# Performance work log

Measured on AMD Instinct MI355X. Metric: run time of the kernel, lower is better.

Reference implementation:

```python
import jax, jax.numpy as jnp
import numpy as np

B, S, D, H = 2, 2048, 1024, 16
HD = D // H  # head_dim = 64


def setup_inputs() -> dict:
    key = jax.random.key(0)
    ks = jax.random.split(key, 9)
    xav = float(np.sqrt(6.0 / (D + D)))  # xavier_uniform bound for square matrices
    def lin_w(k):
        return jax.random.uniform(k, (D, D), jnp.float32, -xav, xav)
    return {
        "x": jax.random.normal(ks[0], (B, S, D), jnp.float32),
        "mask": jnp.ones((B, S), jnp.int32),
        "Wq": lin_w(ks[1]), "bq": jnp.zeros((D,), jnp.float32),
        "Wk": lin_w(ks[2]), "bk": jnp.zeros((D,), jnp.float32),
        "Wv": lin_w(ks[3]), "bv": jnp.zeros((D,), jnp.float32),
        "Wo": lin_w(ks[4]), "bo": jnp.zeros((D,), jnp.float32),
    }


def reference(x, mask, Wq, bq, Wk, bk, Wv, bv, Wo, bo):
    # Linear projections (torch Linear: y = x @ W.T + b)
    q = x @ Wq.T + bq
    k = x @ Wk.T + bk
    v = x @ Wv.T + bv
    # [B, S, D] -> [B, H, S, HD]
    q = q.reshape(B, S, H, HD).transpose(0, 2, 1, 3)
    k = k.reshape(B, S, H, HD).transpose(0, 2, 1, 3)
    v = v.reshape(B, S, H, HD).transpose(0, 2, 1, 3)
    scores = jnp.einsum("bhqd,bhkd->bhqk", q, k) / jnp.sqrt(jnp.float32(HD))
    # mask [B, S] -> [B, 1, 1, S]; masked_fill where mask == 0
    m = mask[:, None, None, :]
    scores = jnp.where(m == 0, jnp.float32(-1e9), scores)
    attn = jax.nn.softmax(scores, axis=-1)
    # dropout in eval mode = identity
    out = jnp.einsum("bhqk,bhkd->bhqd", attn, v)
    out = out.transpose(0, 2, 1, 3).reshape(B, S, D)
    return out @ Wo.T + bo
```

## Files before the change

kernel.cpp:

```cpp
#include <hip/hip_runtime.h>
#include <stdint.h>

#define B_   2
#define S_   2048
#define D_   1024
#define H_   16
#define HD_  64
#define NTOK (B_ * S_)

typedef unsigned short u16;
typedef __bf16 bf16x8 __attribute__((ext_vector_type(8)));
typedef float  f32x4  __attribute__((ext_vector_type(4)));
typedef u16    u16x4  __attribute__((ext_vector_type(4)));
typedef unsigned int u32x2 __attribute__((ext_vector_type(2)));

#define QSCALE 0.180336880f
#define MAXC 4.0f

#if __has_builtin(__builtin_amdgcn_exp2f)
#define EXP2(x) __builtin_amdgcn_exp2f(x)
#else
#define EXP2(x) exp2f(x)
#endif

#define OFF_FLAG ((size_t)0)
#define OFF_BIAS ((size_t)64)
#define OFF_MB   ((size_t)32768)
#define OFF_MF   ((size_t)49152)
#define OFF_X    ((size_t)65536)
#define SZ_X     ((size_t)NTOK * D_ * 2)
#define OFF_W    (OFF_X + SZ_X)
#define SZ_W     ((size_t)D_ * D_ * 2)
#define OFF_Q    (OFF_W + 4 * SZ_W)
#define SZ_T     SZ_X
#define OFF_K2   (OFF_Q + SZ_T)
#define OFF_VT   (OFF_K2 + SZ_T)
#define OFF_AO   (OFF_VT + SZ_T)

__device__ __forceinline__ float bf2f(u16 h) {
    union { uint32_t u; float f; } c; c.u = ((uint32_t)h) << 16; return c.f;
}
__device__ __forceinline__ u16 f2bf(float f) {
    union { float f; uint32_t u; } c; c.f = f;
    uint32_t r = c.u + 0x7fffu + ((c.u >> 16) & 1u);
    return (u16)(r >> 16);
}
__device__ __forceinline__ void glds16(const u16* g, u16* l) {
    __builtin_amdgcn_global_load_lds(
        (const __attribute__((address_space(1))) uint32_t*)g,
        (__attribute__((address_space(3))) uint32_t*)l,
        16, 0, 0);
}
__device__ __forceinline__ f32x4 mfma16(bf16x8 a, bf16x8 b, f32x4 c) {
    return __builtin_amdgcn_mfma_f32_16x16x32_bf16(a, b, c, 0, 0, 0);
}
__device__ __forceinline__ uint32_t pk_bf_trunc(float f0, float f1) {
    return __builtin_amdgcn_perm(__builtin_bit_cast(uint32_t, f1),
                                 __builtin_bit_cast(uint32_t, f0), 0x07060302u);
}
__device__ __forceinline__ void plswap32(uint32_t& a, uint32_t& b) {
#if __has_builtin(__builtin_amdgcn_permlane32_swap)
    u32x2 r = __builtin_amdgcn_permlane32_swap(a, b, false, false);
    a = r[0]; b = r[1];
#else
    asm volatile("s_nop 1\n\tv_permlane32_swap_b32 %0, %1\n\ts_nop 1"
                 : "+v"(a), "+v"(b));
#endif
}
__device__ __forceinline__ void plswap16(uint32_t& a, uint32_t& b) {
#if __has_builtin(__builtin_amdgcn_permlane16_swap)
    u32x2 r = __builtin_amdgcn_permlane16_swap(a, b, false, false);
    a = r[0]; b = r[1];
#else
    asm volatile("s_nop 1\n\tv_permlane16_swap_b32 %0, %1\n\ts_nop 1"
                 : "+v"(a), "+v"(b));
#endif
}

__global__ void convert_kernel(const void* x, const void* wq, const void* wk,
                               const void* wv, const void* wo,
                               const void* bq, const void* bk, const void* bv,
                               const void* bo, const int* mask, char* ws) {
    __shared__ int s_ok;
    const int tid = threadIdx.x;
    if (tid == 0) s_ok = 1;
    __syncthreads();
    {
        const u16* p = (const u16*)wq;
        bool bad = false;
        for (int j = 0; j < 8; ++j) {
            float v = bf2f(p[(tid * 8 + j) * 2]);
            if (!(v > -1.0f && v < 1.0f)) bad = true;
        }
        if (bad) s_ok = 0;
    }
    __syncthreads();
    const int is_bf16 = s_ok;
    if (blockIdx.x == 0 && tid == 0) *(int*)(ws + OFF_FLAG) = is_bf16;

    const uint32_t NX = (uint32_t)NTOK * D_;
    const uint32_t NW = (uint32_t)D_ * D_;
    if (!is_bf16) {
        u16* Xd = (u16*)(ws + OFF_X);
        u16* Wd = (u16*)(ws + OFF_W);
        for (uint32_t i = blockIdx.x * 256u + tid; i < NX + 4 * NW;
             i += gridDim.x * 256u) {
            const void* src; uint32_t si; u16* dst;
            if (i < NX) { src = x; si = i; dst = Xd + i; }
            else {
                uint32_t j = i - NX;
                uint32_t w = j >> 20; si = j & (NW - 1u);
                src = (w == 0) ? wq : (w == 1) ? wk : (w == 2) ? wv : wo;
                dst = Wd + j;
            }
            *dst = f2bf(((const float*)src)[si]);
        }
    }
    float* Bd = (float*)(ws + OFF_BIAS);
    float* Mbd = (float*)(ws + OFF_MB);
    int* MFd = (int*)(ws + OFF_MF);
    const uint32_t NB = 4u * D_;
    const uint32_t total2 = NB + (uint32_t)NTOK + B_ * 32;
    for (uint32_t i = blockIdx.x * 256u + tid; i < total2;
         i += gridDim.x * 256u) {
        if (i < NB) {
            uint32_t w = i >> 10; uint32_t si = i & (D_ - 1u);
            const void* src = (w == 0) ? bq : (w == 1) ? bk : (w == 2) ? bv : bo;
            Bd[i] = is_bf16 ? bf2f(((const u16*)src)[si]) : ((const float*)src)[si];
        } else if (i < NB + (uint32_t)NTOK) {
            uint32_t j = i - NB;
            Mbd[j] = (mask[j] == 0) ? -1.0e9f : 0.0f;
        } else {
            uint32_t f = i - NB - (uint32_t)NTOK;
            uint32_t bb = f >> 5, kt = f & 31;
            int any = 0;
            for (int e = 0; e < 64; ++e)
                any |= (mask[bb * S_ + kt * 64 + e] == 0);
            MFd[f] = any;
        }
    }
}

__global__ void qkv_gemm(char* ws, const void* x, const void* wq,
                         const void* wk, const void* wv) {
    __shared__ alignas(16) u16 As[128 * 32];
    __shared__ alignas(16) u16 Bs[128 * 32];
    const int z = blockIdx.z;
    const int is_bf16 = *(const int*)(ws + OFF_FLAG);
    const u16* X = is_bf16 ? (const u16*)x : (const u16*)(ws + OFF_X);
    const u16* W;
    if (is_bf16) W = (z == 0) ? (const u16*)wq : (z == 1) ? (const u16*)wk : (const u16*)wv;
    else         W = (const u16*)(ws + OFF_W + (size_t)z * SZ_W);
    const float* bias = (const float*)(ws + OFF_BIAS) + z * D_;
    u16* Qd  = (u16*)(ws + OFF_Q);
    u16* Kd  = (u16*)(ws + OFF_K2);
    u16* Vtd = (u16*)(ws + OFF_VT);

    const int tid = threadIdx.x, lane = tid & 63, wave = tid >> 6;
    const int wm = (wave & 1) * 64, wn = (wave >> 1) * 64;
    const int lr = lane & 15, quad = lane >> 4;
    const int srow = tid >> 2;
    const int scol = (((tid & 3) ^ ((tid >> 3) & 3)) * 8);
    const int rd_off = (quad ^ ((lr >> 1) & 3)) * 8;

    const u16* Araw; const u16* Braw; int m0, n0;
    if (z < 2) { Araw = W; Braw = X; m0 = blockIdx.x * 128; n0 = blockIdx.y * 128; }
    else       { Araw = X; Braw = W; m0 = blockIdx.y * 128; n0 = blockIdx.x * 128; }

    f32x4 acc[4][4];
#pragma unroll
    for (int i = 0; i < 4; i++)
#pragma unroll
        for (int j = 0; j < 4; j++) acc[i][j] = (f32x4){0.f, 0.f, 0.f, 0.f};

    const u16* Ag0 = Araw + (size_t)(m0 + srow)      * D_ + scol;
    const u16* Ag1 = Araw + (size_t)(m0 + srow + 64) * D_ + scol;
    const u16* Bg0 = Braw + (size_t)(n0 + srow)      * D_ + scol;
    const u16* Bg1 = Braw + (size_t)(n0 + srow + 64) * D_ + scol;

    for (int k0 = 0; k0 < D_; k0 += 32) {
        glds16(Ag0 + k0, &As[tid * 8]);
        glds16(Ag1 + k0, &As[2048 + tid * 8]);
        glds16(Bg0 + k0, &Bs[tid * 8]);
        glds16(Bg1 + k0, &Bs[2048 + tid * 8]);
        __syncthreads();
        bf16x8 a[4], b[4];
#pragma unroll
        for (int i = 0; i < 4; i++) a[i] = *(const bf16x8*)&As[(wm + i * 16 + lr) * 32 + rd_off];
#pragma unroll
        for (int j = 0; j < 4; j++) b[j] = *(const bf16x8*)&Bs[(wn + j * 16 + lr) * 32 + rd_off];
#pragma unroll
        for (int i = 0; i < 4; i++)
#pragma unroll
            for (int j = 0; j < 4; j++) acc[i][j] = mfma16(a[i], b[j], acc[i][j]);
        __syncthreads();
    }

    if (z < 2) {
        u16* dst0 = (z == 0) ? Qd : Kd;
        const float sc_ = (z == 0) ? QSCALE : 1.0f;
#pragma unroll
        for (int i = 0; i < 4; i++) {
            const int fb = m0 + wm + i * 16 + quad * 4;
            const f32x4 b4 = *(const f32x4*)&bias[fb];
            const int h = fb >> 6, hd0 = fb & 63;
#pragma unroll
            for (int j = 0; j < 4; j++) {
                const int tok = n0 + wn + j * 16 + lr;
                const int bb = tok >> 11, s = tok & 2047;
                u16x4 pk;
#pragma unroll
                for (int r = 0; r < 4; r++) pk[r] = f2bf((acc[i][j][r] + b4[r]) * sc_);
                *(u16x4*)&dst0[(((size_t)(bb * H_ + h)) * S_ + s) * HD_ + hd0] = pk;
            }
        }
    } else {
#pragma unroll
        for (int i = 0; i < 4; i++) {
            const int row_b = m0 + wm + i * 16 + quad * 4;
            const int bb = row_b >> 11, s0 = row_b & 2047;
#pragma unroll
            for (int j = 0; j < 4; j++) {
                const int col = n0 + wn + j * 16 + lr;
                const float bv_ = bias[col];
                const int h = col >> 6, hd = col & 63;
                u16x4 pk;
#pragma unroll
                for (int r = 0; r < 4; r++) pk[r] = f2bf(acc[i][j][r] + bv_);
                *(u16x4*)&Vtd[(((size_t)(bb * H_ + h)) * HD_ + hd) * S_ + s0] = pk;
            }
        }
    }
}

__global__ void __launch_bounds__(256, 2)
attn_kernel(char* ws) {
    __shared__ alignas(16) char smem[32768];

    const u16* Qb  = (const u16*)(ws + OFF_Q);
    const u16* Kb  = (const u16*)(ws + OFF_K2);
    const u16* Vtb = (const u16*)(ws + OFF_VT);
    const float* Mb = (const float*)(ws + OFF_MB);
    const int* MF = (const int*)(ws + OFF_MF);
    u16* AO = (u16*)(ws + OFF_AO);

    const int tid = threadIdx.x, lane = tid & 63, wave = tid >> 6;
    const int lin = blockIdx.x;
    const int work = (lin & 7) * 64 + (lin >> 3);
    const int bh = work >> 4, b = bh >> 4, h = bh & 15;
    const int qb = (work & 15) * 128 + wave * 32;
    const int lr = lane & 15, quad = lane >> 4;
    const int sx = lr & 7;

    const u16* Qbh = Qb  + (size_t)bh * S_ * HD_;
    const u16* Kbh = Kb  + (size_t)bh * S_ * HD_;
    const u16* Vbh = Vtb + (size_t)bh * HD_ * S_;
    const float* Mbb = Mb + b * S_;
    const int* MFb = MF + b * 32;

    u16* Ks0  = (u16*)(smem);
    u16* Vts0 = (u16*)(smem + 8192);
    u16* Ks1  = (u16*)(smem + 16384);
    u16* Vts1 = (u16*)(smem + 24576);

    const int st_r = tid >> 3;
    const int st_c = (tid & 7) ^ (st_r & 7);
    const u16* Kst = Kbh + (size_t)st_r * HD_ + st_c * 8;
    const u16* Vst = Vbh + (size_t)st_r * S_ + st_c * 8;

    bf16x8 qf[2][2];
#pragma unroll
    for (int s = 0; s < 2; ++s)
#pragma unroll
        for (int hf = 0; hf < 2; ++hf)
            qf[s][hf] = *(const bf16x8*)&Qbh[(size_t)(qb + s * 16 + lr) * HD_ + hf * 32 + quad * 8];

    bf16x8 ones8;
#pragma unroll
    for (int i = 0; i < 8; ++i) ones8[i] = (__bf16)1.0f;

    const f32x4 initm = (f32x4){-MAXC, -MAXC, -MAXC, -MAXC};

    f32x4 oacc[2][4], lacc[2];
#pragma unroll
    for (int s = 0; s < 2; ++s) {
        lacc[s] = (f32x4){0.f, 0.f, 0.f, 0.f};
#pragma unroll
        for (int j = 0; j < 4; ++j) oacc[s][j] = (f32x4){0.f, 0.f, 0.f, 0.f};
    }

    auto STAGE = [&](int it2, u16* Kd, u16* Vd) {
        const u16* kg = Kst + (size_t)it2 * 64 * HD_;
        const u16* vg = Vst + it2 * 64;
#pragma unroll
        for (int t = 0; t < 2; ++t) {
            glds16(kg + (size_t)t * 32 * HD_, &Kd[(t * 256 + tid) * 8]);
            glds16(vg + (size_t)t * 32 * S_,  &Vd[(t * 256 + tid) * 8]);
        }
    };

    auto COMPUTE = [&](int it, const u16* Ks, const u16* Vts) {
        const int k0 = it * 64;
        f32x4 sc[2][4];
        __builtin_amdgcn_s_setprio(1);
#pragma unroll
        for (int j = 0; j < 4; ++j) {
            const int krow = (j * 16 + lr) * 64;
            bf16x8 kfA = *(const bf16x8*)&Ks[krow + ((quad    ) ^ sx) * 8];
            bf16x8 kfB = *(const bf16x8*)&Ks[krow + ((quad + 4) ^ sx) * 8];
#pragma unroll
            for (int s = 0; s < 2; ++s) {
                f32x4 t0 = mfma16(kfA, qf[s][0], initm);
                sc[s][j] = mfma16(kfB, qf[s][1], t0);
            }
        }
        __builtin_amdgcn_s_setprio(0);
        if (MFb[it]) {
#pragma unroll
            for (int j = 0; j < 4; ++j) {
                const f32x4 mb = *(const f32x4*)&Mbb[k0 + j * 16 + quad * 4];
#pragma unroll
                for (int s = 0; s < 2; ++s) sc[s][j] += mb;
            }
        }
        bf16x8 vf[4][2];
#pragma unroll
        for (int j2 = 0; j2 < 4; ++j2) {
            const int vrow = (j2 * 16 + lr) * 64;
            vf[j2][0] = *(const bf16x8*)&Vts[vrow + ((quad    ) ^ sx) * 8];
            vf[j2][1] = *(const bf16x8*)&Vts[vrow + ((quad + 4) ^ sx) * 8];
        }

#pragma unroll
        for (int s = 0; s < 2; ++s) {
            uint32_t ulo[4], uhi[4];
#pragma unroll
            for (int j = 0; j < 4; ++j) {
                f32x4 p;
#pragma unroll
                for (int r = 0; r < 4; ++r) p[r] = EXP2(sc[s][j][r]);
                ulo[j] = pk_bf_trunc(p[0], p[1]);
                uhi[j] = pk_bf_trunc(p[2], p[3]);
            }
            bf16x8 pf[2];
#pragma unroll
            for (int half = 0; half < 2; ++half) {
                uint32_t x0 = ulo[2 * half], y0 = ulo[2 * half + 1];
                uint32_t x1 = uhi[2 * half], y1 = uhi[2 * half + 1];
                plswap32(x0, y0); plswap16(x0, y0);
                plswap32(x1, y1); plswap16(x1, y1);
                union { uint32_t u[4]; bf16x8 v; } cvt;
                cvt.u[0] = x0;
                cvt.u[1] = x1;
                cvt.u[2] = y0;
                cvt.u[3] = y1;
                pf[half] = cvt.v;
            }
            __builtin_amdgcn_s_setprio(1);
            lacc[s] = mfma16(ones8, pf[0], lacc[s]);
            lacc[s] = mfma16(ones8, pf[1], lacc[s]);
#pragma unroll
            for (int j2 = 0; j2 < 4; ++j2) {
                oacc[s][j2] = mfma16(vf[j2][0], pf[0], oacc[s][j2]);
                oacc[s][j2] = mfma16(vf[j2][1], pf[1], oacc[s][j2]);
            }
            __builtin_amdgcn_s_setprio(0);
        }
    };

    STAGE(0, Ks0, Vts0);
    for (int itp = 0; itp < 16; ++itp) {
        const int itA = 2 * itp, itB = 2 * itp + 1;
        __syncthreads();
        STAGE(itB, Ks1, Vts1);
        COMPUTE(itA, Ks0, Vts0);
        __syncthreads();
        if (itA + 2 < 32) STAGE(itA + 2, Ks0, Vts0);
        COMPUTE(itB, Ks1, Vts1);
    }

#pragma unroll
    for (int s = 0; s < 2; ++s) {
        const float linv = 1.0f / lacc[s][0];
        const int q = qb + s * 16 + lr;
        u16* dst = AO + (size_t)(b * S_ + q) * D_ + h * HD_ + quad * 4;
#pragma unroll
        for (int j2 = 0; j2 < 4; ++j2) {
            u16x4 pk;
#pragma unroll
            for (int r = 0; r < 4; ++r) pk[r] = f2bf(oacc[s][j2][r] * linv);
            *(u16x4*)&dst[j2 * 16] = pk;
        }
    }
}

__global__ void out_gemm(char* ws, const void* wo, void* dout) {
    __shared__ alignas(16) u16 As[128 * 32];
    __shared__ alignas(16) u16 Bs[64 * 32];
    const int is_bf16 = *(const int*)(ws + OFF_FLAG);
    const u16* A  = (const u16*)(ws + OFF_AO);
    const u16* Bt = is_bf16 ? (const u16*)wo : (const u16*)(ws + OFF_W + 3 * SZ_W);
    const float* bias = (const float*)(ws + OFF_BIAS) + 3 * D_;

    const int tid = threadIdx.x, lane = tid & 63, wave = tid >> 6;
    const int wm = (wave & 1) * 64, wn = (wave >> 1) * 32;
    const int m0 = blockIdx.y * 128, n0 = blockIdx.x * 64;
    const int lr = lane & 15, quad = lane >> 4;
    const int srow = tid >> 2;
    const int scol = (((tid & 3) ^ ((tid >> 3) & 3)) * 8);
    const int rd_off = (quad ^ ((lr >> 1) & 3)) * 8;

    f32x4 acc[4][2];
#pragma unroll
    for (int i = 0; i < 4; i++)
#pragma unroll
        for (int j = 0; j < 2; j++) acc[i][j] = (f32x4){0.f, 0.f, 0.f, 0.f};

    const u16* Ag0 = A  + (size_t)(m0 + srow)      * D_ + scol;
    const u16* Ag1 = A  + (size_t)(m0 + srow + 64) * D_ + scol;
    const u16* Bg0 = Bt + (size_t)(n0 + srow)      * D_ + scol;

    for (int k0 = 0; k0 < D_; k0 += 32) {
        glds16(Ag0 + k0, &As[tid * 8]);
        glds16(Ag1 + k0, &As[2048 + tid * 8]);
        glds16(Bg0 + k0, &Bs[tid * 8]);
        __syncthreads();
        bf16x8 a[4], b[2];
#pragma unroll
        for (int i = 0; i < 4; i++) a[i] = *(const bf16x8*)&As[(wm + i * 16 + lr) * 32 + rd_off];
#pragma unroll
        for (int j = 0; j < 2; j++) b[j] = *(const bf16x8*)&Bs[(wn + j * 16 + lr) * 32 + rd_off];
#pragma unroll
        for (int i = 0; i < 4; i++)
#pragma unroll
            for (int j = 0; j < 2; j++) acc[i][j] = mfma16(a[i], b[j], acc[i][j]);
        __syncthreads();
    }
#pragma unroll
    for (int i = 0; i < 4; i++) {
        const int row_b = m0 + wm + i * 16 + quad * 4;
#pragma unroll
        for (int j = 0; j < 2; j++) {
            const int col = n0 + wn + j * 16 + lr;
            const float bv_ = bias[col];
#pragma unroll
            for (int r = 0; r < 4; r++) {
                const int row = row_b + r;
                const float v = acc[i][j][r] + bv_;
                const size_t idx = (size_t)row * D_ + col;
                if (is_bf16) ((u16*)dout)[idx] = f2bf(v);
                else         ((float*)dout)[idx] = v;
            }
        }
    }
}

extern "C" void kernel_launch(void* const* d_in, const int* in_sizes, int n_in,
                              void* d_out, int out_size, void* d_ws, size_t ws_size,
                              hipStream_t stream) {
    (void)in_sizes; (void)n_in; (void)out_size; (void)ws_size;
    const void* x  = d_in[0];
    const int* mask = (const int*)d_in[1];
    const void* wq = d_in[2]; const void* bq = d_in[3];
    const void* wk = d_in[4]; const void* bk = d_in[5];
    const void* wv = d_in[6]; const void* bv = d_in[7];
    const void* wo = d_in[8]; const void* bo = d_in[9];
    char* ws = (char*)d_ws;

    convert_kernel<<<dim3(2048), dim3(256), 0, stream>>>(x, wq, wk, wv, wo,
                                                         bq, bk, bv, bo, mask, ws);
    qkv_gemm<<<dim3(8, 32, 3), dim3(256), 0, stream>>>(ws, x, wq, wk, wv);
    attn_kernel<<<dim3(512), dim3(256), 0, stream>>>(ws);
    out_gemm<<<dim3(16, 32), dim3(256), 0, stream>>>(ws, wo, d_out);
}
```

Before: 206.5 us.

## Double-buffer LDS in projection GEMMs, remap blocks per XCD, vectorize output stores

Both projection GEMMs now use two LDS buffers, so the global-to-LDS loads for the next K slice are issued while the current slice is computed. The loop is unrolled by two and drops one barrier per K step. Blocks are launched on a flat grid and remapped so consecutive blocks on the same XCD share token tiles, which is meant to improve L2 reuse. out_gemm swaps operand roles (Wo as A, activations as B) so the epilogue can write vectorized 4-wide rows with a vector bias load. Launch bounds are added, and the doubled LDS may limit occupancy.

```diff
diff --git a/kernel.cpp b/kernel.cpp
--- a/kernel.cpp
+++ b/kernel.cpp
@@ -141,11 +141,17 @@
     }
 }
 
-__global__ void qkv_gemm(char* ws, const void* x, const void* wq,
-                         const void* wk, const void* wv) {
-    __shared__ alignas(16) u16 As[128 * 32];
-    __shared__ alignas(16) u16 Bs[128 * 32];
-    const int z = blockIdx.z;
+__global__ void __launch_bounds__(256, 3)
+qkv_gemm(char* ws, const void* x, const void* wq,
+         const void* wk, const void* wv) {
+    __shared__ alignas(16) u16 As[2][128 * 32];
+    __shared__ alignas(16) u16 Bs[2][128 * 32];
+    const int lin = blockIdx.x;
+    const int xcd = lin & 7, slot = lin >> 3;
+    const int zx = slot >> 2, ly = slot & 3;
+    const int z = zx >> 3, xt = zx & 7;
+    const int yt = xcd * 4 + ly;
+
     const int is_bf16 = *(const int*)(ws + OFF_FLAG);
     const u16* X = is_bf16 ? (const u16*)x : (const u16*)(ws + OFF_X);
     const u16* W;
@@ -164,8 +170,8 @@
     const int rd_off = (quad ^ ((lr >> 1) & 3)) * 8;
 
     const u16* Araw; const u16* Braw; int m0, n0;
-    if (z < 2) { Araw = W; Braw = X; m0 = blockIdx.x * 128; n0 = blockIdx.y * 128; }
-    else       { Araw = X; Braw = W; m0 = blockIdx.y * 128; n0 = blockIdx.x * 128; }
+    if (z < 2) { Araw = W; Braw = X; m0 = xt * 128; n0 = yt * 128; }
+    else       { Araw = X; Braw = W; m0 = yt * 128; n0 = xt * 128; }
 
     f32x4 acc[4][4];
 #pragma unroll
@@ -178,22 +184,32 @@
     const u16* Bg0 = Braw + (size_t)(n0 + srow)      * D_ + scol;
     const u16* Bg1 = Braw + (size_t)(n0 + srow + 64) * D_ + scol;
 
-    for (int k0 = 0; k0 < D_; k0 += 32) {
-        glds16(Ag0 + k0, &As[tid * 8]);
-        glds16(Ag1 + k0, &As[2048 + tid * 8]);
-        glds16(Bg0 + k0, &Bs[tid * 8]);
-        glds16(Bg1 + k0, &Bs[2048 + tid * 8]);
+    auto STAGE = [&](int k0, u16* Ad, u16* Bd2) {
+        glds16(Ag0 + k0, &Ad[tid * 8]);
+        glds16(Ag1 + k0, &Ad[2048 + tid * 8]);
+        glds16(Bg0 + k0, &Bd2[tid * 8]);
+        glds16(Bg1 + k0, &Bd2[2048 + tid * 8]);
+    };
+    auto COMPUTE = [&](const u16* Ad, const u16* Bd2) {
+        bf16x8 a[4], b[4];
+#pragma unroll
+        for (int i = 0; i < 4; i++) a[i] = *(const bf16x8*)&Ad[(wm + i * 16 + lr) * 32 + rd_off];
+#pragma unroll
+        for (int j = 0; j < 4; j++) b[j] = *(const bf16x8*)&Bd2[(wn + j * 16 + lr) * 32 + rd_off];
+#pragma unroll
+        for (int i = 0; i < 4; i++)
+#pragma unroll
+            for (int j = 0; j < 4; j++) acc[i][j] = mfma16(a[i], b[j], acc[i][j]);
+    };
+
+    STAGE(0, As[0], Bs[0]);
+    for (int kp = 0; kp < 16; ++kp) {
         __syncthreads();
-        bf16x8 a[4], b[4];
-#pragma unroll
-        for (int i = 0; i < 4; i++) a[i] = *(const bf16x8*)&As[(wm + i * 16 + lr) * 32 + rd_off];
-#pragma unroll
-        for (int j = 0; j < 4; j++) b[j] = *(const bf16x8*)&Bs[(wn + j * 16 + lr) * 32 + rd_off];
-#pragma unroll
-        for (int i = 0; i < 4; i++)
-#pragma unroll
-            for (int j = 0; j < 4; j++) acc[i][j] = mfma16(a[i], b[j], acc[i][j]);
+        STAGE(kp * 64 + 32, As[1], Bs[1]);
+        COMPUTE(As[0], Bs[0]);
         __syncthreads();
+        if (kp < 15) STAGE(kp * 64 + 64, As[0], Bs[0]);
+        COMPUTE(As[1], Bs[1]);
     }
 
     if (z < 2) {
@@ -394,17 +410,23 @@
     }
 }
 
-__global__ void out_gemm(char* ws, const void* wo, void* dout) {
-    __shared__ alignas(16) u16 As[128 * 32];
-    __shared__ alignas(16) u16 Bs[64 * 32];
+__global__ void __launch_bounds__(256, 2)
+out_gemm(char* ws, const void* wo, void* dout) {
+    __shared__ alignas(16) u16 As[2][128 * 32];
+    __shared__ alignas(16) u16 Bs[2][64 * 32];
     const int is_bf16 = *(const int*)(ws + OFF_FLAG);
-    const u16* A  = (const u16*)(ws + OFF_AO);
-    const u16* Bt = is_bf16 ? (const u16*)wo : (const u16*)(ws + OFF_W + 3 * SZ_W);
+    const u16* A  = is_bf16 ? (const u16*)wo : (const u16*)(ws + OFF_W + 3 * SZ_W);
+    const u16* Bt = (const u16*)(ws + OFF_AO);
     const float* bias = (const float*)(ws + OFF_BIAS) + 3 * D_;
+
+    const int lin = blockIdx.x;
+    const int xcd = lin & 7, slot = lin >> 3;
+    const int ty = xcd * 8 + (slot >> 3);
+    const int fx = slot & 7;
+    const int m0 = fx * 128, n0 = ty * 64;
 
     const int tid = threadIdx.x, lane = tid & 63, wave = tid >> 6;
     const int wm = (wave & 1) * 64, wn = (wave >> 1) * 32;
-    const int m0 = blockIdx.y * 128, n0 = blockIdx.x * 64;
     const int lr = lane & 15, quad = lane >> 4;
     const int srow = tid >> 2;
     const int scol = (((tid & 3) ^ ((tid >> 3) & 3)) * 8);
@@ -420,36 +442,51 @@
     const u16* Ag1 = A  + (size_t)(m0 + srow + 64) * D_ + scol;
     const u16* Bg0 = Bt + (size_t)(n0 + srow)      * D_ + scol;
 
-    for (int k0 = 0; k0 < D_; k0 += 32) {
-        glds16(Ag0 + k0, &As[tid * 8]);
-        glds16(Ag1 + k0, &As[2048 + tid * 8]);
-        glds16(Bg0 + k0, &Bs[tid * 8]);
+    auto STAGE = [&](int k0, u16* Ad, u16* Bd2) {
+        glds16(Ag0 + k0, &Ad[tid * 8]);
+        glds16(Ag1 + k0, &Ad[2048 + tid * 8]);
+        glds16(Bg0 + k0, &Bd2[tid * 8]);
+    };
+    auto COMPUTE = [&](const u16* Ad, const u16* Bd2) {
+        bf16x8 a[4], b[2];
+#pragma unroll
+        for (int i = 0; i < 4; i++) a[i] = *(const bf16x8*)&Ad[(wm + i * 16 + lr) * 32 + rd_off];
+#pragma unroll
+        for (int j = 0; j < 2; j++) b[j] = *(const bf16x8*)&Bd2[(wn + j * 16 + lr) * 32 + rd_off];
+#pragma unroll
+        for (int i = 0; i < 4; i++)
+#pragma unroll
+            for (int j = 0; j < 2; j++) acc[i][j] = mfma16(a[i], b[j], acc[i][j]);
+    };
+
+    STAGE(0, As[0], Bs[0]);
+    for (int kp = 0; kp < 16; ++kp) {
         __syncthreads();
-        bf16x8 a[4], b[2];
-#pragma unroll
-        for (int i = 0; i < 4; i++) a[i] = *(const bf16x8*)&As[(wm + i * 16 + lr) * 32 + rd_off];
-#pragma unroll
-        for (int j = 0; j < 2; j++) b[j] = *(const bf16x8*)&Bs[(wn + j * 16 + lr) * 32 + rd_off];
-#pragma unroll
-        for (int i = 0; i < 4; i++)
-#pragma unroll
-            for (int j = 0; j < 2; j++) acc[i][j] = mfma16(a[i], b[j], acc[i][j]);
+        STAGE(kp * 64 + 32, As[1], Bs[1]);
+        COMPUTE(As[0], Bs[0]);
         __syncthreads();
-    }
+        if (kp < 15) STAGE(kp * 64 + 64, As[0], Bs[0]);
+        COMPUTE(As[1], Bs[1]);
+    }
+
 #pragma unroll
     for (int i = 0; i < 4; i++) {
-        const int row_b = m0 + wm + i * 16 + quad * 4;
+        const int fb = m0 + wm + i * 16 + quad * 4;
+        const f32x4 b4 = *(const f32x4*)&bias[fb];
 #pragma unroll
         for (int j = 0; j < 2; j++) {
-            const int col = n0 + wn + j * 16 + lr;
-            const float bv_ = bias[col];
-#pragma unroll
-            for (int r = 0; r < 4; r++) {
-                const int row = row_b + r;
-                const float v = acc[i][j][r] + bv_;
-                const size_t idx = (size_t)row * D_ + col;
-                if (is_bf16) ((u16*)dout)[idx] = f2bf(v);
-                else         ((float*)dout)[idx] = v;
+            const int tok = n0 + wn + j * 16 + lr;
+            const size_t idx = (size_t)tok * D_ + fb;
+            if (is_bf16) {
+                u16x4 pk;
+#pragma unroll
+                for (int r = 0; r < 4; r++) pk[r] = f2bf(acc[i][j][r] + b4[r]);
+                *(u16x4*)&((u16*)dout)[idx] = pk;
+            } else {
+                f32x4 v4;
+#pragma unroll
+                for (int r = 0; r < 4; r++) v4[r] = acc[i][j][r] + b4[r];
+                *(f32x4*)&((float*)dout)[idx] = v4;
             }
         }
     }
@@ -469,7 +506,7 @@
 
     convert_kernel<<<dim3(2048), dim3(256), 0, stream>>>(x, wq, wk, wv, wo,
                                                          bq, bk, bv, bo, mask, ws);
-    qkv_gemm<<<dim3(8, 32, 3), dim3(256), 0, stream>>>(ws, x, wq, wk, wv);
+    qkv_gemm<<<dim3(768), dim3(256), 0, stream>>>(ws, x, wq, wk, wv);
     attn_kernel<<<dim3(512), dim3(256), 0, stream>>>(ws);
-    out_gemm<<<dim3(16, 32), dim3(256), 0, stream>>>(ws, wo, d_out);
-}
+    out_gemm<<<dim3(512), dim3(256), 0, stream>>>(ws, wo, d_out);
+}
```

Result: faster. 201.0 us (-2.7%).
